# Kernel tuning notes

Measured on AMD Instinct MI355X. Metric: run time of the kernel, lower is better.

## Reference

```python
import jax, jax.numpy as jnp
import numpy as np

N_NODES = 100000
N_EDGES = 1000000
N_RELS = 8
N_HEADS = 4
IN_FEAT = 64
OUT_FEAT = 64
D_HEAD = OUT_FEAT // N_HEADS
LEAKY_SLOPE = 0.2


def setup_inputs() -> dict:
    key = jax.random.key(0)
    ks = jax.random.split(key, 8)
    x = jax.random.normal(ks[0], (N_NODES, IN_FEAT), dtype=jnp.float32)
    src_idx = jax.random.randint(ks[1], (N_EDGES,), 0, N_NODES)
    dst_idx = jax.random.randint(ks[2], (N_EDGES,), 0, N_NODES)
    edge_rel = jnp.sort(jax.random.randint(ks[3], (N_EDGES,), 0, N_RELS))
    # xavier-ish small init for weights
    conv_weights = jax.random.normal(ks[4], (N_RELS, N_HEADS, IN_FEAT, D_HEAD), dtype=jnp.float32) * 0.1
    attn_l = jax.random.normal(ks[5], (N_RELS, N_HEADS, D_HEAD), dtype=jnp.float32) * 0.1
    attn_r = jax.random.normal(ks[6], (N_RELS, N_HEADS, D_HEAD), dtype=jnp.float32) * 0.1
    h_bias = jnp.zeros((OUT_FEAT,), dtype=jnp.float32)
    return {
        'x': x, 'src_idx': src_idx, 'dst_idx': dst_idx, 'edge_rel': edge_rel,
        'conv_weights': conv_weights, 'attn_l': attn_l, 'attn_r': attn_r,
        'h_bias': h_bias,
    }


def reference(x, src_idx, dst_idx, edge_rel, conv_weights, attn_l, attn_r, h_bias):
    N = x.shape[0]
    # Per-relation transform of all node features: [R, N, H, D]
    feat_all = jnp.einsum('ni,rhid->rnhd', x, conv_weights)
    # Per-relation attention logits per node: [R, N, H]
    el_all = jnp.einsum('rnhd,rhd->rnh', feat_all, attn_l)
    er_all = jnp.einsum('rnhd,rhd->rnh', feat_all, attn_r)
    # Gather per-edge quantities (relation-specific transform of src/dst)
    feat_e = feat_all[edge_rel, src_idx]          # [E, H, D]
    el = el_all[edge_rel, src_idx]                # [E, H]
    er = er_all[edge_rel, dst_idx]                # [E, H]
    s = jax.nn.leaky_relu(el + er, negative_slope=LEAKY_SLOPE)
    # Edge softmax over incoming edges of each destination node (per head)
    m = jax.ops.segment_max(s, dst_idx, num_segments=N)      # [N, H]
    e = jnp.exp(s - m[dst_idx])                               # [E, H]
    denom = jax.ops.segment_sum(e, dst_idx, num_segments=N)   # [N, H]
    w = e / jnp.maximum(denom[dst_idx], jnp.float32(1e-16))   # [E, H]
    # Weighted aggregation of source features into destination nodes
    agg = jax.ops.segment_sum(feat_e * w[..., None], dst_idx, num_segments=N)  # [N, H, D]
    h = agg.reshape(N, OUT_FEAT) + h_bias
    # activation=None, dropout in eval mode -> identity
    return h
```

## Files before the change

### kernel.cpp

```cpp
#include <hip/hip_runtime.h>
#include <hip/hip_bf16.h>

#define NN 100000
#define NE 1000000
#define NR 8

#define EB 1024
#define NBLK 977
#define NBUCK 196
#define NT (NBUCK*NBLK)
#define NBB 749

#define K3DPB 32
#define K3CAP 160

#define K1RPB 2
#define K1GROUPS (NR / K1RPB)

#define K0_BLKS  160
#define PRE_BLKS (K0_BLKS + NBLK)

typedef unsigned short u16;
typedef unsigned int u32;
typedef __attribute__((ext_vector_type(8))) short bf16x8;
typedef __attribute__((ext_vector_type(4))) float f32x4;

static __device__ __forceinline__ float bf2f(u16 u) {
    union { u32 i; float f; } v; v.i = ((u32)u) << 16; return v.f;
}
static __device__ __forceinline__ float bflo(u32 u) {
    union { u32 i; float f; } v; v.i = u << 16; return v.f;
}
static __device__ __forceinline__ float bfhi(u32 u) {
    union { u32 i; float f; } v; v.i = u & 0xffff0000u; return v.f;
}
static __device__ __forceinline__ u16 f2bf(float f) {
    __hip_bfloat16 h = __float2bfloat16(f);
    return *reinterpret_cast<u16*>(&h);
}
static __device__ __forceinline__ float ldf(const void* p, int idx, int isf32) {
    return isf32 ? ((const float*)p)[idx] : bf2f(((const u16*)p)[idx]);
}

static __device__ __forceinline__ int detect_wave(const u16* xw, int lane)
{
    int insane = 0;
    for (int k = lane; k < 512; k += 64) {
        u16 w = xw[k];
        int ex = (w >> 7) & 0xFF;
        bool sane = ((w & 0x7FFF) == 0) || (ex >= 96 && ex <= 159);
        insane += sane ? 0 : 1;
    }
    for (int off = 32; off; off >>= 1) insane += __shfl_down(insane, off);
    return insane;
}

__global__ __launch_bounds__(256) void k_pre(
    const void* __restrict__ xin, int* __restrict__ flag,
    const void* __restrict__ cw, const void* __restrict__ al,
    const void* __restrict__ ar, u16* __restrict__ Bpre,
    const int* __restrict__ dsti, int* __restrict__ histT)
{
    __shared__ int sflag;
    __shared__ int hist[NBUCK];
    int t = threadIdx.x;
    int b = blockIdx.x;

    if (b < K0_BLKS) {
        if (t < 64) {
            int insane = detect_wave((const u16*)xin, t);
            if (t == 0) {
                sflag = (insane > 50) ? 1 : 0;
                if (b == 0) *flag = sflag;
            }
        }
        __syncthreads();
        int isf32 = sflag;
        int tid = b * 256 + t;
        if (tid >= NR * 5120) return;
        int r = tid / 5120, rem = tid % 5120;
        int c = rem >> 3, j = rem & 7;
        int nt = c >> 7, kk = (c >> 6) & 1, lc = c & 63;
        int i = kk * 32 + ((lc >> 4) << 3) + j;
        int d = lc & 15;
        u16 val;
        if (nt < 4) {
            val = f2bf(ldf(cw, ((r * 4 + nt) * 64 + i) * 16 + d, isf32));
        } else if (d < 8) {
            int h = d >> 1;
            const void* attn = (d & 1) ? ar : al;
            float s = 0.f;
            for (int dd = 0; dd < 16; ++dd)
                s += ldf(cw, ((r * 4 + h) * 64 + i) * 16 + dd, isf32)
                   * ldf(attn, (r * 4 + h) * 16 + dd, isf32);
            val = f2bf(s);
        } else {
            val = 0;
        }
        Bpre[tid] = val;
    } else {
        int blk = b - K0_BLKS;
        if (t < NBUCK) hist[t] = 0;
        __syncthreads();
        int base = blk * EB;
        for (int j = 0; j < EB; j += 256) {
            int e = base + j + t;
            if (e < NE) atomicAdd(&hist[dsti[e] >> 9], 1);
        }
        __syncthreads();
        if (t < NBUCK) histT[t * NBLK + blk] = hist[t];
    }
}

__global__ __launch_bounds__(256) void k1_feat(
    const void* __restrict__ xin, const u16* __restrict__ Bpre,
    u16* __restrict__ feat_all, float* __restrict__ el_all, float* __restrict__ er_all)
{
    __shared__ u32 ldsT[K1RPB][64][32];
    int chunk = blockIdx.x >> 2;
    int r0 = (blockIdx.x & 3) * K1RPB;
    int n0 = chunk * 64;
    int tid = threadIdx.x;
    int wave = tid >> 6, lane = tid & 63;
    int col = lane & 15, quad = lane >> 4;

    int insane = detect_wave((const u16*)xin, lane);
    insane = __shfl(insane, 0);
    int isf32 = (insane > 50) ? 1 : 0;

    int node = n0 + wave * 16 + col;
    int nclamp = node < NN ? node : NN - 1;
    bool nvalid = node < NN;

    bf16x8 afrag0, afrag1;
    if (!isf32) {
        const u16* xb = (const u16*)xin + nclamp * 64 + quad * 8;
        afrag0 = *(const bf16x8*)&xb[0];
        afrag1 = *(const bf16x8*)&xb[32];
    } else {
        const float* xf = (const float*)xin + nclamp * 64 + quad * 8;
#pragma unroll
        for (int j = 0; j < 8; ++j) {
            afrag0[j] = (short)f2bf(xf[j]);
            afrag1[j] = (short)f2bf(xf[32 + j]);
        }
    }

#pragma unroll
    for (int rr = 0; rr < K1RPB; ++rr) {
        int r = r0 + rr;
        f32x4 acc[5];
#pragma unroll
        for (int nt = 0; nt < 5; ++nt) acc[nt] = f32x4{0.f, 0.f, 0.f, 0.f};
#pragma unroll
        for (int nt = 0; nt < 5; ++nt) {
            bf16x8 b0 = *(const bf16x8*)&Bpre[r * 5120 + ((nt * 2 + 0) * 64 + lane) * 8];
            bf16x8 b1 = *(const bf16x8*)&Bpre[r * 5120 + ((nt * 2 + 1) * 64 + lane) * 8];
            acc[nt] = __builtin_amdgcn_mfma_f32_16x16x32_bf16(b0, afrag0, acc[nt], 0, 0, 0);
            acc[nt] = __builtin_amdgcn_mfma_f32_16x16x32_bf16(b1, afrag1, acc[nt], 0, 0, 0);
        }

#pragma unroll
        for (int nt = 0; nt < 4; ++nt) {
            u32 lo = (u32)f2bf(acc[nt][0]) | ((u32)f2bf(acc[nt][1]) << 16);
            u32 hi = (u32)f2bf(acc[nt][2]) | ((u32)f2bf(acc[nt][3]) << 16);
            int w = (nt * 8 + quad * 2) ^ (col * 2);
            *(uint2*)&ldsT[rr][wave * 16 + col][w] = uint2{lo, hi};
        }
        if (nvalid && quad < 2) {
            int eb = (r * NN + node) * 4 + quad * 2;
            *(float2*)&el_all[eb] = float2{acc[4][0], acc[4][2]};
            *(float2*)&er_all[eb] = float2{acc[4][1], acc[4][3]};
        }
    }
    __syncthreads();

#pragma unroll
    for (int it = 0; it < K1RPB * 4; ++it) {
        int u = it * 256 + tid;
        int rr = u >> 10;
        int v = u & 1023;
        int nl = v >> 4;
        int p  = v & 15;
        int w  = (p * 2) ^ ((nl & 15) * 2);
        uint2 val = *(const uint2*)&ldsT[rr][nl][w];
        int nd = n0 + nl;
        if (nd < NN)
            *(uint2*)&feat_all[((r0 + rr) * NN + nd) * 64 + p * 4] = val;
    }
}

__global__ __launch_bounds__(256) void k_scanB1(int* __restrict__ histT,
                                                int* __restrict__ bsum)
{
    __shared__ int wtot[4];
    int t = threadIdx.x;
    int gi = blockIdx.x * 256 + t;
    int v = (gi < NT) ? histT[gi] : 0;
    int lane = t & 63, w = t >> 6;
    int s = v;
#pragma unroll
    for (int m = 1; m < 64; m <<= 1) {
        int u = __shfl_up(s, m);
        if (lane >= m) s += u;
    }
    if (lane == 63) wtot[w] = s;
    __syncthreads();
    int wb = 0;
    for (int i = 0; i < w; ++i) wb += wtot[i];
    if (gi < NT) histT[gi] = wb + s - v;
    if (t == 255) bsum[blockIdx.x] = wb + s;
}

__global__ __launch_bounds__(1024) void k_scanB2(const int* __restrict__ bsum,
                                                 int* __restrict__ boff,
                                                 const int* __restrict__ histT,
                                                 int* __restrict__ bstart)
{
    __shared__ int wtot[16];
    __shared__ int sboff[NBB];
    int t = threadIdx.x;
    int v = (t < NBB) ? bsum[t] : 0;
    int lane = t & 63, w = t >> 6;
    int s = v;
#pragma unroll
    for (int m = 1; m < 64; m <<= 1) {
        int u = __shfl_up(s, m);
        if (lane >= m) s += u;
    }
    if (lane == 63) wtot[w] = s;
    __syncthreads();
    int wb = 0;
    for (int i = 0; i < w; ++i) wb += wtot[i];
    if (t < NBB) {
        int val = wb + s - v;
        boff[t] = val;
        sboff[t] = val;
    }
    __syncthreads();
    if (t < NBUCK) {
        int gi = t * NBLK;
        bstart[t] = histT[gi] + sboff[gi >> 8];
    }
    if (t == 0) bstart[NBUCK] = NE;
}

__global__ __launch_bounds__(256) void k_binC(
    const int* __restrict__ srci, const int* __restrict__ dsti,
    const int* __restrict__ reli, const int* __restrict__ histT,
    const int* __restrict__ boff, int* __restrict__ key_b)
{
    __shared__ int cur[NBUCK];
    int t = threadIdx.x, blk = blockIdx.x;
    if (t < NBUCK) {
        int gi = t * NBLK + blk;
        cur[t] = histT[gi] + boff[gi >> 8];
    }
    __syncthreads();
    int base = blk * EB;
    for (int j = 0; j < EB; j += 256) {
        int e = base + j + t;
        if (e < NE) {
            int d = dsti[e];
            int key = ((d & 511) << 20) | (reli[e] << 17) | srci[e];
            int pos = atomicAdd(&cur[d >> 9], 1);
            key_b[pos] = key;
        }
    }
}

__global__ __launch_bounds__(1024) void k_binD(
    const int* __restrict__ bstart, const int* __restrict__ key_b,
    int* __restrict__ key_s, int* __restrict__ off)
{
    __shared__ int cnt[512];
    __shared__ int wtot[8];
    int t = threadIdx.x, b = blockIdx.x;
    int s0 = bstart[b], s1 = bstart[b + 1];
    if (t < 512) cnt[t] = 0;
    __syncthreads();
    for (int j = s0 + t; j < s1; j += 1024)
        atomicAdd(&cnt[(key_b[j] >> 20) & 511], 1);
    __syncthreads();
    int excl = 0;
    if (t < 512) {
        int v = cnt[t];
        int lane = t & 63, w = t >> 6;
        int s = v;
#pragma unroll
        for (int m = 1; m < 64; m <<= 1) {
            int u = __shfl_up(s, m);
            if (lane >= m) s += u;
        }
        if (lane == 63) wtot[w] = s;
        __syncthreads();
        int wb = 0;
        for (int i = 0; i < w; ++i) wb += wtot[i];
        excl = s0 + wb + s - v;
        int d = (b << 9) + t;
        if (d < NN) off[d] = excl;
    } else {
        __syncthreads();
    }
    __syncthreads();
    if (t < 512) cnt[t] = excl;
    if (b == 0 && t == 0) off[NN] = NE;
    __syncthreads();
    for (int j = s0 + t; j < s1; j += 1024) {
        int key = key_b[j];
        int pos = atomicAdd(&cnt[(key >> 20) & 511], 1);
        key_s[pos] = key;
    }
}

__global__ __launch_bounds__(256) void k3_node(
    const int* __restrict__ off, const int* __restrict__ key_s,
    const float* __restrict__ el_all, const float* __restrict__ er_all,
    const u16* __restrict__ feat_all, const void* __restrict__ bias,
    const int* __restrict__ flag, void* __restrict__ out)
{
    __shared__ int   ldsOffs[K3DPB + 1];
    __shared__ int   ldsKey[4][K3CAP];
    __shared__ float ldsEE[4][K3CAP][4];
    int t = threadIdx.x;
    int wave = t >> 6, lane = t & 63;
    int dg = lane >> 3;
    int fl = lane & 7;
    int h  = fl >> 1;
    int d0 = blockIdx.x * K3DPB;
    int isf32 = *flag;

    if (t < K3DPB + 1) ldsOffs[t] = off[min(d0 + t, NN)];
    __syncthreads();

    int dlo = wave * 8;
    int estart = ldsOffs[dlo], eend = ldsOffs[dlo + 8];
    int scount = min(eend - estart, K3CAP);

    int dbase = d0 & ~511;
    for (int j = lane; j < scount; j += 64) {
        int key = key_s[estart + j];
        int rel = (key >> 17) & 7, src = key & 131071;
        int d = dbase | ((key >> 20) & 511);
        int kk = rel * NN + src;
        f32x4 el = *(const f32x4*)&el_all[kk * 4];
        f32x4 er = *(const f32x4*)&er_all[(rel * NN + d) * 4];
        f32x4 ee;
#pragma unroll
        for (int q = 0; q < 4; ++q) {
            float v = el[q] + er[q];
            v = v > 0.f ? v : 0.2f * v;
            ee[q] = __expf(v);
        }
        ldsKey[wave][j] = kk;
        *(f32x4*)&ldsEE[wave][j][0] = ee;
    }

    float bv[8];
#pragma unroll
    for (int q = 0; q < 8; ++q) bv[q] = ldf(bias, fl * 8 + q, isf32);

    int nl = dlo + dg;
    int d = d0 + nl;
    int s  = ldsOffs[nl] - estart;
    int e1 = ldsOffs[nl + 1] - estart;
    float acc[8] = {0.f, 0.f, 0.f, 0.f, 0.f, 0.f, 0.f, 0.f};
    float accW = 0.f;

    int e1c = min(e1, K3CAP);
    for (int base = s; base < e1c; base += 4) {
        int kk[4]; float w[4];
#pragma unroll
        for (int q = 0; q < 4; ++q) {
            int idx = base + q;
            bool vld = idx < e1c;
            kk[q] = vld ? ldsKey[wave][idx] : 0;
            w[q]  = vld ? ldsEE[wave][idx][h] : 0.f;
        }
        uint4 u[4];
#pragma unroll
        for (int q = 0; q < 4; ++q)
            u[q] = *(const uint4*)&feat_all[kk[q] * 64 + fl * 8];
#pragma unroll
        for (int q = 0; q < 4; ++q) {
            acc[0] += bflo(u[q].x) * w[q];
            acc[1] += bfhi(u[q].x) * w[q];
            acc[2] += bflo(u[q].y) * w[q];
            acc[3] += bfhi(u[q].y) * w[q];
            acc[4] += bflo(u[q].z) * w[q];
            acc[5] += bfhi(u[q].z) * w[q];
            acc[6] += bflo(u[q].w) * w[q];
            acc[7] += bfhi(u[q].w) * w[q];
            accW += w[q];
        }
    }
    for (int j = max(s, K3CAP); j < e1; ++j) {
        int key = key_s[estart + j];
        int rel = (key >> 17) & 7, src = key & 131071;
        int kk0 = rel * NN + src;
        float v = el_all[kk0 * 4 + h] + er_all[(rel * NN + d) * 4 + h];
        v = v > 0.f ? v : 0.2f * v;
        float w0 = __expf(v);
        uint4 u = *(const uint4*)&feat_all[kk0 * 64 + fl * 8];
        acc[0] += bflo(u.x) * w0;
        acc[1] += bfhi(u.x) * w0;
        acc[2] += bflo(u.y) * w0;
        acc[3] += bfhi(u.y) * w0;
        acc[4] += bflo(u.z) * w0;
        acc[5] += bfhi(u.z) * w0;
        acc[6] += bflo(u.w) * w0;
        acc[7] += bfhi(u.w) * w0;
        accW += w0;
    }

    {
        float invh = 1.f / fmaxf(accW, 1e-16f);
        float o[8];
#pragma unroll
        for (int q = 0; q < 8; ++q) o[q] = acc[q] * invh + bv[q];
        if (isf32) {
            ((f32x4*)out)[d * 16 + fl * 2]     = f32x4{o[0], o[1], o[2], o[3]};
            ((f32x4*)out)[d * 16 + fl * 2 + 1] = f32x4{o[4], o[5], o[6], o[7]};
        } else {
            uint4 st;
            st.x = (u32)f2bf(o[0]) | ((u32)f2bf(o[1]) << 16);
            st.y = (u32)f2bf(o[2]) | ((u32)f2bf(o[3]) << 16);
            st.z = (u32)f2bf(o[4]) | ((u32)f2bf(o[5]) << 16);
            st.w = (u32)f2bf(o[6]) | ((u32)f2bf(o[7]) << 16);
            *(uint4*)&((u16*)out)[d * 64 + fl * 8] = st;
        }
    }
}

extern "C" void kernel_launch(void* const* d_in, const int* in_sizes, int n_in,
                              void* d_out, int out_size, void* d_ws, size_t ws_size,
                              hipStream_t stream)
{
    const void* x   = d_in[0];
    const int* srci = (const int*)d_in[1];
    const int* dsti = (const int*)d_in[2];
    const int* reli = (const int*)d_in[3];
    const void* cw  = d_in[4];
    const void* al  = d_in[5];
    const void* ar  = d_in[6];
    const void* hb  = d_in[7];

    char* ws = (char*)d_ws;
    u16*   feat_all = (u16*)  (ws + 0);
    float* el_all   = (float*)(ws + 102400000);
    float* er_all   = (float*)(ws + 115200000);
    int*   key_s    = (int*)  (ws + 128000000);
    int*   key_b    = (int*)  (ws + 132000000);
    int*   off      = (int*)  (ws + 136000000);
    int*   histT    = (int*)  (ws + 136400064);
    int*   bsum     = (int*)  (ws + 137166032);
    int*   boff     = (int*)  (ws + 137169040);
    int*   bstart   = (int*)  (ws + 137172048);
    u16*   Bpre     = (u16*)  (ws + 137172880);
    int*   flag     = (int*)  (ws + 137254800);

    k_pre<<<PRE_BLKS, 256, 0, stream>>>(x, flag, cw, al, ar, Bpre, dsti, histT);
    k1_feat<<<((NN + 63) / 64) * K1GROUPS, 256, 0, stream>>>(x, Bpre, feat_all, el_all, er_all);
    k_scanB1<<<NBB, 256, 0, stream>>>(histT, bsum);
    k_scanB2<<<1, 1024, 0, stream>>>(bsum, boff, histT, bstart);
    k_binC<<<NBLK, 256, 0, stream>>>(srci, dsti, reli, histT, boff, key_b);
    k_binD<<<NBUCK, 1024, 0, stream>>>(bstart, key_b, key_s, off);
    k3_node<<<(NN + 31) / 32, 256, 0, stream>>>(off, key_s, el_all, er_all, feat_all,
                                                hb, flag, d_out);
}
```

Before: 212.7 us.

## Skip writing unused (relation, source) feature rows via an edge-built bitmap

The pre-pass now sets a bit in a relation-by-node bitmap for every (relation, source) pair that appears on an edge. The feature kernel writes a node's transformed feature row only when its bit is set, so feature rows no edge ever reads are never stored. The feature kernel also now handles four relations per block instead of two, with the relation loop no longer unrolled. The aggregation kernel's padding lanes now read an already-fetched key instead of row 0. The cost is one memset plus global atomicOr traffic in the pre-pass and a bitmap read per store.

```diff
diff --git a/kernel.cpp b/kernel.cpp
--- a/kernel.cpp
+++ b/kernel.cpp
@@ -14,7 +14,7 @@
 #define K3DPB 32
 #define K3CAP 160
 
-#define K1RPB 2
+#define K1RPB 4
 #define K1GROUPS (NR / K1RPB)
 
 #define K0_BLKS  160
@@ -59,7 +59,9 @@
     const void* __restrict__ xin, int* __restrict__ flag,
     const void* __restrict__ cw, const void* __restrict__ al,
     const void* __restrict__ ar, u16* __restrict__ Bpre,
-    const int* __restrict__ dsti, int* __restrict__ histT)
+    const int* __restrict__ dsti, const int* __restrict__ srci,
+    const int* __restrict__ reli, u32* __restrict__ srcmap,
+    int* __restrict__ histT)
 {
     __shared__ int sflag;
     __shared__ int hist[NBUCK];
@@ -105,7 +107,12 @@
         int base = blk * EB;
         for (int j = 0; j < EB; j += 256) {
             int e = base + j + t;
-            if (e < NE) atomicAdd(&hist[dsti[e] >> 9], 1);
+            if (e < NE) {
+                int d = dsti[e];
+                atomicAdd(&hist[d >> 9], 1);
+                int kk = reli[e] * NN + srci[e];
+                atomicOr(&srcmap[kk >> 5], 1u << (kk & 31));
+            }
         }
         __syncthreads();
         if (t < NBUCK) histT[t * NBLK + blk] = hist[t];
@@ -114,11 +121,12 @@
 
 __global__ __launch_bounds__(256) void k1_feat(
     const void* __restrict__ xin, const u16* __restrict__ Bpre,
+    const u32* __restrict__ srcmap,
     u16* __restrict__ feat_all, float* __restrict__ el_all, float* __restrict__ er_all)
 {
     __shared__ u32 ldsT[K1RPB][64][32];
-    int chunk = blockIdx.x >> 2;
-    int r0 = (blockIdx.x & 3) * K1RPB;
+    int chunk = blockIdx.x >> 1;
+    int r0 = (blockIdx.x & 1) * K1RPB;
     int n0 = chunk * 64;
     int tid = threadIdx.x;
     int wave = tid >> 6, lane = tid & 63;
@@ -146,7 +154,7 @@
         }
     }
 
-#pragma unroll
+#pragma unroll 1
     for (int rr = 0; rr < K1RPB; ++rr) {
         int r = r0 + rr;
         f32x4 acc[5];
@@ -182,11 +190,13 @@
         int v = u & 1023;
         int nl = v >> 4;
         int p  = v & 15;
+        int nd = n0 + nl;
+        if (nd >= NN) continue;
+        int kk = (r0 + rr) * NN + nd;
+        if (!((srcmap[kk >> 5] >> (kk & 31)) & 1)) continue;
         int w  = (p * 2) ^ ((nl & 15) * 2);
         uint2 val = *(const uint2*)&ldsT[rr][nl][w];
-        int nd = n0 + nl;
-        if (nd < NN)
-            *(uint2*)&feat_all[((r0 + rr) * NN + nd) * 64 + p * 4] = val;
+        *(uint2*)&feat_all[kk * 64 + p * 4] = val;
     }
 }
 
@@ -374,7 +384,7 @@
         for (int q = 0; q < 4; ++q) {
             int idx = base + q;
             bool vld = idx < e1c;
-            kk[q] = vld ? ldsKey[wave][idx] : 0;
+            kk[q] = vld ? ldsKey[wave][idx] : ldsKey[wave][base];
             w[q]  = vld ? ldsEE[wave][idx][h] : 0.f;
         }
         uint4 u[4];
@@ -458,9 +468,13 @@
     int*   bstart   = (int*)  (ws + 137172048);
     u16*   Bpre     = (u16*)  (ws + 137172880);
     int*   flag     = (int*)  (ws + 137254800);
-
-    k_pre<<<PRE_BLKS, 256, 0, stream>>>(x, flag, cw, al, ar, Bpre, dsti, histT);
-    k1_feat<<<((NN + 63) / 64) * K1GROUPS, 256, 0, stream>>>(x, Bpre, feat_all, el_all, er_all);
+    u32*   srcmap   = (u32*)  (ws + 137254816);
+
+    hipMemsetAsync(srcmap, 0, 100000, stream);
+    k_pre<<<PRE_BLKS, 256, 0, stream>>>(x, flag, cw, al, ar, Bpre,
+                                        dsti, srci, reli, srcmap, histT);
+    k1_feat<<<((NN + 63) / 64) * K1GROUPS, 256, 0, stream>>>(x, Bpre, srcmap,
+                                                             feat_all, el_all, er_all);
     k_scanB1<<<NBB, 256, 0, stream>>>(histT, bsum);
     k_scanB2<<<1, 1024, 0, stream>>>(bsum, boff, histT, bstart);
     k_binC<<<NBLK, 256, 0, stream>>>(srci, dsti, reli, histT, boff, key_b);
```

After: 250.0 us. 1.18x slower.
